# Optimization experiments

Hardware: AMD Instinct MI355X
Metric: run time of the kernel (lower is better)

Reference implementation:

```python
import jax, jax.numpy as jnp
import numpy as np

P_THRESH = 20  # p=0.2 * 100
# direction -> (di, dj): masked pixel (i,j) writes input[i,j] to x[i+di, j+dj], then avg to x[i,j]
OFFSETS = {0: (-1, -1), 1: (-1, 0), 2: (-1, 1), 3: (0, -1), 4: (0, 0), 5: (0, 1), 6: (1, -1), 7: (1, 0)}


def _shift(a, di, dj):
    """out[i+di, j+dj] = a[i, j] on last two axes; out-of-range -> 0/False."""
    H, W = a.shape[-2], a.shape[-1]
    pad = [(0, 0)] * (a.ndim - 2) + [(max(di, 0), max(-di, 0)), (max(dj, 0), max(-dj, 0))]
    p = jnp.pad(a, pad)
    sh, sw = max(-di, 0), max(-dj, 0)
    return p[..., sh:sh + H, sw:sw + W]


def _avg3x3_reflect(x):
    H, W = x.shape[-2], x.shape[-1]
    p = jnp.pad(x, [(0, 0), (0, 0), (1, 1), (1, 1)], mode='reflect')
    s = jnp.zeros_like(x)
    for i in range(3):
        for j in range(3):
            s = s + p[..., i:i + H, j:j + W]
    return s / 9.0


def brown_forward(input, dir, prob):
    avg = _avg3x3_reflect(input)
    pos = prob <= P_THRESH
    x = input
    for d in range(8):  # sequential, matching torch in-place write order
        di, dj = OFFSETS[d]
        m = (dir == d) & pos
        if d == 4:
            x = jnp.where(m, avg, x)  # mm: only avg write
        else:
            sm = _shift(m, di, dj)                       # neighbor-target mask
            x = jnp.where(sm, _shift(input, di, dj), x)  # x[i+di,j+dj] = input[i,j]
            mv = _shift(sm, -di, -dj)                    # mask restricted to valid region
            x = jnp.where(mv, avg, x)                    # x[i,j] = avg[i,j]
    return x


def setup_inputs() -> dict:
    key = jax.random.key(0)
    k1, k2, k3 = jax.random.split(key, 3)
    shape = (32, 64, 128, 128)
    return {
        'input': jax.random.normal(k1, shape, dtype=jnp.float32),
        'dir': jax.random.randint(k2, shape, 0, 8, dtype=jnp.int32),
        'prob': jax.random.randint(k3, shape, 1, 100, dtype=jnp.int32),
    }


def reference(input, dir, prob):
    return brown_forward(input, dir, prob)
```

## Files before the change

### kernel.cpp

```cpp
#include <hip/hip_runtime.h>
#include <cstddef>

#define H 128
#define W 128
#define TILE_R 32
#define P_THRESH 20

__global__ __launch_bounds__(256, 6)
void brown_kernel(const float* __restrict__ inp,
                  const int*  __restrict__ dirp,
                  const int*  __restrict__ prb,
                  float* __restrict__ out)
{
    const int tid   = threadIdx.x;
    const int bid   = blockIdx.x;
    const int slice = bid >> 2;
    const int r0    = (bid & 3) * TILE_R;
    const size_t base = (size_t)slice * (size_t)(H * W);

    const int cq  = tid & 31;
    const int rg  = tid >> 5;
    const int j0  = cq << 2;
    const int gi0 = r0 + (rg << 2);

    auto load_row = [&](int k, float v[6], unsigned& ma, unsigned& mb) {
        const int gr  = gi0 - 1 + k;
        const int gri = (gr < 0) ? 1 : ((gr >= H) ? (H - 2) : gr);
        const float4 c = ((const float4*)(inp + base + (size_t)gri * W))[cq];
        unsigned mwc;
        if ((unsigned)gr < (unsigned)H) {
            const int4 dv = ((const int4*)(dirp + base + (size_t)gr * W))[cq];
            const int4 pv = ((const int4*)(prb  + base + (size_t)gr * W))[cq];
            const unsigned a  = (pv.x <= P_THRESH) ? (unsigned)dv.x : 8u;
            const unsigned b  = (pv.y <= P_THRESH) ? (unsigned)dv.y : 8u;
            const unsigned cc = (pv.z <= P_THRESH) ? (unsigned)dv.z : 8u;
            const unsigned d  = (pv.w <= P_THRESH) ? (unsigned)dv.w : 8u;
            mwc = a | (b << 8) | (cc << 16) | (d << 24);
        } else {
            mwc = 0x08080808u;
        }
        const float    lf  = __shfl_up(c.w, 1);
        const float    rt  = __shfl_down(c.x, 1);
        const unsigned mwl = __shfl_up(mwc, 1);
        const unsigned mwr = __shfl_down(mwc, 1);
        v[1] = c.x; v[2] = c.y; v[3] = c.z; v[4] = c.w;
        v[0] = (cq > 0)  ? lf : c.y;
        v[5] = (cq < 31) ? rt : c.z;
        const unsigned ml = (cq > 0)  ? (mwl >> 24)  : 8u;
        const unsigned mr = (cq < 31) ? (mwr & 255u) : 8u;
        ma = (mwc << 8) | ml;
        mb = (mwc >> 8) | (mr << 24);
    };

    float va[6], vb[6], vc[6];
    unsigned maa, mab, mba, mbb, mca, mcb;
    load_row(0, va, maa, mab);
    load_row(1, vb, mba, mbb);

    #pragma unroll
    for (int rr = 0; rr < 4; ++rr) {
        load_row(rr + 2, vc, mca, mcb);

        const int gi = gi0 + rr;
        float cs[6];
        #pragma unroll
        for (int w = 0; w < 6; ++w) cs[w] = va[w] + vb[w] + vc[w];

        float4 res;
        float* rp = (float*)&res;
        #pragma unroll
        for (int p = 0; p < 4; ++p) {
            const float avg = (cs[p] + cs[p + 1] + cs[p + 2]) * (1.0f / 9.0f);
            const unsigned wTop = (p < 2) ? (maa >> (8 * p)) : (mab >> (8 * (p - 2)));
            const unsigned wMid = (p < 2) ? (mba >> (8 * p)) : (mbb >> (8 * (p - 2)));
            const unsigned wBot = (p < 2) ? (mca >> (8 * p)) : (mcb >> (8 * (p - 2)));

            float val = vb[p + 1];
            int dl = -1;
            if (((wBot >> 16) & 255u) == 0u) { val = vc[p + 2]; dl = 0; }
            if (((wBot >>  8) & 255u) == 1u) { val = vc[p + 1]; dl = 1; }
            if (( wBot        & 255u) == 2u) { val = vc[p];     dl = 2; }
            if (((wMid >> 16) & 255u) == 3u) { val = vb[p + 2]; dl = 3; }
            if (( wMid        & 255u) == 5u) { val = vb[p];     dl = 5; }
            if (((wTop >> 16) & 255u) == 6u) { val = va[p + 2]; dl = 6; }
            if (((wTop >>  8) & 255u) == 7u) { val = va[p + 1]; dl = 7; }

            const int msel = (int)((wMid >> 8) & 255u);
            const int q3 = (msel * 11) >> 5;
            const int di = q3 - 1;
            const int dj = msel - q3 * 3 - 1;
            const int ti = gi + di;
            const int tj = j0 + p + dj;
            const bool bok = (msel < 8) & ((unsigned)ti < 128u) & ((unsigned)tj < 128u);
            if (bok & (msel >= dl)) val = avg;
            rp[p] = val;
        }
        ((float4*)(out + base + (size_t)gi * W))[cq] = res;

        #pragma unroll
        for (int w = 0; w < 6; ++w) { va[w] = vb[w]; vb[w] = vc[w]; }
        maa = mba; mab = mbb; mba = mca; mbb = mcb;
    }
}

extern "C" void kernel_launch(void* const* d_in, const int* in_sizes, int n_in,
                              void* d_out, int out_size, void* d_ws, size_t ws_size,
                              hipStream_t stream) {
    const float* inp  = (const float*)d_in[0];
    const int*   dirp = (const int*)d_in[1];
    const int*   prb  = (const int*)d_in[2];
    float* out = (float*)d_out;

    const int slices = in_sizes[0] / (H * W);
    const int grid = slices * (H / TILE_R);
    brown_kernel<<<grid, 256, 0, stream>>>(inp, dirp, prb, out);
}
```

Measured before the change: 405.6 us.

## Batch all window row loads upfront, use 8 rows per thread and nontemporal stores

Each thread now handles 8 output rows instead of 4, and each block covers 64 rows instead of 32, which cuts the halo re-read overhead from 6/4 to 10/8 rows. All input, dir and prob loads for the 10-row window are issued up front, so more memory requests are in flight before any compute starts. Output is written with nontemporal stores. The cost is higher register pressure (launch bounds lowered to 4 blocks per SM) and half as many blocks in the grid.

Result: faster. 396.0 us (-2.4%).

```diff
diff --git a/kernel.cpp b/kernel.cpp
--- a/kernel.cpp
+++ b/kernel.cpp
@@ -3,10 +3,13 @@
 
 #define H 128
 #define W 128
-#define TILE_R 32
+#define ROWS 8
+#define WIN (ROWS + 2)
 #define P_THRESH 20
 
-__global__ __launch_bounds__(256, 6)
+typedef float nf4 __attribute__((ext_vector_type(4)));
+
+__global__ __launch_bounds__(256, 4)
 void brown_kernel(const float* __restrict__ inp,
                   const int*  __restrict__ dirp,
                   const int*  __restrict__ prb,
@@ -14,20 +17,27 @@
 {
     const int tid   = threadIdx.x;
     const int bid   = blockIdx.x;
-    const int slice = bid >> 2;
-    const int r0    = (bid & 3) * TILE_R;
+    const int slice = bid >> 1;
+    const int r0    = (bid & 1) << 6;
     const size_t base = (size_t)slice * (size_t)(H * W);
 
     const int cq  = tid & 31;
     const int rg  = tid >> 5;
     const int j0  = cq << 2;
-    const int gi0 = r0 + (rg << 2);
+    const int gi0 = r0 + rg * ROWS;
 
-    auto load_row = [&](int k, float v[6], unsigned& ma, unsigned& mb) {
+    float4 c[WIN];
+    #pragma unroll
+    for (int k = 0; k < WIN; ++k) {
         const int gr  = gi0 - 1 + k;
         const int gri = (gr < 0) ? 1 : ((gr >= H) ? (H - 2) : gr);
-        const float4 c = ((const float4*)(inp + base + (size_t)gri * W))[cq];
-        unsigned mwc;
+        c[k] = ((const float4*)(inp + base + (size_t)gri * W))[cq];
+    }
+
+    unsigned mw[WIN];
+    #pragma unroll
+    for (int k = 0; k < WIN; ++k) {
+        const int gr = gi0 - 1 + k;
         if ((unsigned)gr < (unsigned)H) {
             const int4 dv = ((const int4*)(dirp + base + (size_t)gr * W))[cq];
             const int4 pv = ((const int4*)(prb  + base + (size_t)gr * W))[cq];
@@ -35,39 +45,49 @@
             const unsigned b  = (pv.y <= P_THRESH) ? (unsigned)dv.y : 8u;
             const unsigned cc = (pv.z <= P_THRESH) ? (unsigned)dv.z : 8u;
             const unsigned d  = (pv.w <= P_THRESH) ? (unsigned)dv.w : 8u;
-            mwc = a | (b << 8) | (cc << 16) | (d << 24);
+            mw[k] = a | (b << 8) | (cc << 16) | (d << 24);
         } else {
-            mwc = 0x08080808u;
+            mw[k] = 0x08080808u;
         }
-        const float    lf  = __shfl_up(c.w, 1);
-        const float    rt  = __shfl_down(c.x, 1);
-        const unsigned mwl = __shfl_up(mwc, 1);
-        const unsigned mwr = __shfl_down(mwc, 1);
-        v[1] = c.x; v[2] = c.y; v[3] = c.z; v[4] = c.w;
-        v[0] = (cq > 0)  ? lf : c.y;
-        v[5] = (cq < 31) ? rt : c.z;
+    }
+
+    float lf[WIN], rt[WIN];
+    unsigned ma[WIN], mb[WIN];
+    #pragma unroll
+    for (int k = 0; k < WIN; ++k) {
+        const float    l   = __shfl_up(c[k].w, 1);
+        const float    r   = __shfl_down(c[k].x, 1);
+        const unsigned mwl = __shfl_up(mw[k], 1);
+        const unsigned mwr = __shfl_down(mw[k], 1);
+        lf[k] = (cq > 0)  ? l : c[k].y;
+        rt[k] = (cq < 31) ? r : c[k].z;
         const unsigned ml = (cq > 0)  ? (mwl >> 24)  : 8u;
         const unsigned mr = (cq < 31) ? (mwr & 255u) : 8u;
-        ma = (mwc << 8) | ml;
-        mb = (mwc >> 8) | (mr << 24);
-    };
-
-    float va[6], vb[6], vc[6];
-    unsigned maa, mab, mba, mbb, mca, mcb;
-    load_row(0, va, maa, mab);
-    load_row(1, vb, mba, mbb);
+        ma[k] = (mw[k] << 8) | ml;
+        mb[k] = (mw[k] >> 8) | (mr << 24);
+    }
 
     #pragma unroll
-    for (int rr = 0; rr < 4; ++rr) {
-        load_row(rr + 2, vc, mca, mcb);
+    for (int rr = 0; rr < ROWS; ++rr) {
+        const int gi = gi0 + rr;
 
-        const int gi = gi0 + rr;
+        float va[6], vb[6], vc[6];
+        va[0] = lf[rr];     va[1] = c[rr].x;   va[2] = c[rr].y;
+        va[3] = c[rr].z;    va[4] = c[rr].w;   va[5] = rt[rr];
+        vb[0] = lf[rr+1];   vb[1] = c[rr+1].x; vb[2] = c[rr+1].y;
+        vb[3] = c[rr+1].z;  vb[4] = c[rr+1].w; vb[5] = rt[rr+1];
+        vc[0] = lf[rr+2];   vc[1] = c[rr+2].x; vc[2] = c[rr+2].y;
+        vc[3] = c[rr+2].z;  vc[4] = c[rr+2].w; vc[5] = rt[rr+2];
+
         float cs[6];
         #pragma unroll
         for (int w = 0; w < 6; ++w) cs[w] = va[w] + vb[w] + vc[w];
 
-        float4 res;
-        float* rp = (float*)&res;
+        const unsigned maa = ma[rr],   mab = mb[rr];
+        const unsigned mba = ma[rr+1], mbb = mb[rr+1];
+        const unsigned mca = ma[rr+2], mcb = mb[rr+2];
+
+        nf4 res;
         #pragma unroll
         for (int p = 0; p < 4; ++p) {
             const float avg = (cs[p] + cs[p + 1] + cs[p + 2]) * (1.0f / 9.0f);
@@ -93,13 +113,9 @@
             const int tj = j0 + p + dj;
             const bool bok = (msel < 8) & ((unsigned)ti < 128u) & ((unsigned)tj < 128u);
             if (bok & (msel >= dl)) val = avg;
-            rp[p] = val;
+            res[p] = val;
         }
-        ((float4*)(out + base + (size_t)gi * W))[cq] = res;
-
-        #pragma unroll
-        for (int w = 0; w < 6; ++w) { va[w] = vb[w]; vb[w] = vc[w]; }
-        maa = mba; mab = mbb; mba = mca; mbb = mcb;
+        __builtin_nontemporal_store(res, (nf4*)(out + base + (size_t)gi * W) + cq);
     }
 }
 
@@ -112,6 +128,6 @@
     float* out = (float*)d_out;
 
     const int slices = in_sizes[0] / (H * W);
-    const int grid = slices * (H / TILE_R);
+    const int grid = slices * 2;
     brown_kernel<<<grid, 256, 0, stream>>>(inp, dirp, prb, out);
 }
```

## Stage per-wave row tiles in LDS via direct global-to-LDS loads

Applied to the files above, without the earlier changes.

Each wave now loads a 10-row halo tile of input into LDS with global_load_lds and packs the direction/probability masks into LDS, instead of having every thread reload overlapping rows and exchange mask bytes through shuffles. Each half-wave then computes 4 output rows from LDS, and output is written with nontemporal stores. The aim is to cut redundant global reads of halo rows (from 6 loaded rows per 4 output rows down to 10 per 8 per wave) and to issue all loads up front for more memory-level parallelism. In exchange it adds LDS traffic and a wait on all outstanding loads before compute. It also relies on global_load_lds landing data at the expected per-lane offsets with no barrier, which is safe only because each wave reads only its own LDS region.

Measured after the change: 392.6 us. 1.03x faster.

```diff
diff --git a/kernel.cpp b/kernel.cpp
--- a/kernel.cpp
+++ b/kernel.cpp
@@ -3,8 +3,13 @@
 
 #define H 128
 #define W 128
-#define TILE_R 32
+#define WROWS 8
+#define LROWS 10
 #define P_THRESH 20
+
+typedef float nf4 __attribute__((ext_vector_type(4)));
+typedef __attribute__((address_space(1))) const unsigned int glo_u32;
+typedef __attribute__((address_space(3))) unsigned int lds_u32;
 
 __global__ __launch_bounds__(256, 6)
 void brown_kernel(const float* __restrict__ inp,
@@ -12,37 +17,71 @@
                   const int*  __restrict__ prb,
                   float* __restrict__ out)
 {
+    __shared__ __align__(16) float s_in[4 * LROWS * W];
+    __shared__ unsigned int        s_mk[4 * LROWS * 32];
+
     const int tid   = threadIdx.x;
+    const int wid   = tid >> 6;
+    const int lane  = tid & 63;
     const int bid   = blockIdx.x;
     const int slice = bid >> 2;
-    const int r0    = (bid & 3) * TILE_R;
+    const int r0    = (bid & 3) << 5;
+    const int wr0   = r0 + wid * WROWS;
     const size_t base = (size_t)slice * (size_t)(H * W);
 
-    const int cq  = tid & 31;
-    const int rg  = tid >> 5;
-    const int j0  = cq << 2;
-    const int gi0 = r0 + (rg << 2);
+    float*        s_in_w = s_in + wid * (LROWS * W);
+    unsigned int* s_mk_w = s_mk + wid * (LROWS * 32);
 
-    auto load_row = [&](int k, float v[6], unsigned& ma, unsigned& mb) {
-        const int gr  = gi0 - 1 + k;
+    int4 dvv[5], pvv[5];
+    #pragma unroll
+    for (int w = 0; w < 5; ++w) {
+        const int idx = w * 64 + lane;
+        const int L   = idx >> 5;
+        const int c4  = idx & 31;
+        const int gr  = wr0 - 1 + L;
+        if ((unsigned)gr < (unsigned)H) {
+            dvv[w] = ((const int4*)(dirp + base + (size_t)gr * W))[c4];
+            pvv[w] = ((const int4*)(prb  + base + (size_t)gr * W))[c4];
+        } else {
+            dvv[w] = make_int4(8, 8, 8, 8);
+            pvv[w] = make_int4(100, 100, 100, 100);
+        }
+    }
+    #pragma unroll
+    for (int w = 0; w < 5; ++w) {
+        const int idx = w * 64 + lane;
+        const int L   = idx >> 5;
+        const int c4  = idx & 31;
+        const int gr  = wr0 - 1 + L;
         const int gri = (gr < 0) ? 1 : ((gr >= H) ? (H - 2) : gr);
-        const float4 c = ((const float4*)(inp + base + (size_t)gri * W))[cq];
-        unsigned mwc;
-        if ((unsigned)gr < (unsigned)H) {
-            const int4 dv = ((const int4*)(dirp + base + (size_t)gr * W))[cq];
-            const int4 pv = ((const int4*)(prb  + base + (size_t)gr * W))[cq];
-            const unsigned a  = (pv.x <= P_THRESH) ? (unsigned)dv.x : 8u;
-            const unsigned b  = (pv.y <= P_THRESH) ? (unsigned)dv.y : 8u;
-            const unsigned cc = (pv.z <= P_THRESH) ? (unsigned)dv.z : 8u;
-            const unsigned d  = (pv.w <= P_THRESH) ? (unsigned)dv.w : 8u;
-            mwc = a | (b << 8) | (cc << 16) | (d << 24);
-        } else {
-            mwc = 0x08080808u;
-        }
-        const float    lf  = __shfl_up(c.w, 1);
-        const float    rt  = __shfl_down(c.x, 1);
-        const unsigned mwl = __shfl_up(mwc, 1);
-        const unsigned mwr = __shfl_down(mwc, 1);
+        const float* gp = inp + base + (size_t)gri * W + c4 * 4;
+        __builtin_amdgcn_global_load_lds((glo_u32*)gp, (lds_u32*)(s_in_w + idx * 4), 16, 0, 0);
+    }
+    #pragma unroll
+    for (int w = 0; w < 5; ++w) {
+        const int idx = w * 64 + lane;
+        const unsigned a  = (pvv[w].x <= P_THRESH) ? (unsigned)dvv[w].x : 8u;
+        const unsigned b  = (pvv[w].y <= P_THRESH) ? (unsigned)dvv[w].y : 8u;
+        const unsigned cc = (pvv[w].z <= P_THRESH) ? (unsigned)dvv[w].z : 8u;
+        const unsigned d  = (pvv[w].w <= P_THRESH) ? (unsigned)dvv[w].w : 8u;
+        s_mk_w[idx] = a | (b << 8) | (cc << 16) | (d << 24);
+    }
+    asm volatile("s_waitcnt vmcnt(0)" ::: "memory");
+
+    const int cq   = lane & 31;
+    const int rh   = lane >> 6 ? 0 : (lane >> 5);
+    const int j0   = cq << 2;
+    const int lrb  = rh << 2;
+    const int cqm1 = (cq > 0)  ? cq - 1 : 0;
+    const int cqp1 = (cq < 31) ? cq + 1 : 31;
+
+    auto load_row = [&](int L, float v[6], unsigned& ma, unsigned& mb) {
+        const float4   c   = ((const float4*)(s_in_w + L * W))[cq];
+        const unsigned mwc = s_mk_w[L * 32 + cq];
+        const unsigned mwl = s_mk_w[L * 32 + cqm1];
+        const unsigned mwr = s_mk_w[L * 32 + cqp1];
+        const float lf = __shfl_up(c.w, 1);
+        const float rt = __shfl_down(c.x, 1);
         v[1] = c.x; v[2] = c.y; v[3] = c.z; v[4] = c.w;
         v[0] = (cq > 0)  ? lf : c.y;
         v[5] = (cq < 31) ? rt : c.z;
@@ -54,20 +93,19 @@
 
     float va[6], vb[6], vc[6];
     unsigned maa, mab, mba, mbb, mca, mcb;
-    load_row(0, va, maa, mab);
-    load_row(1, vb, mba, mbb);
+    load_row(lrb + 0, va, maa, mab);
+    load_row(lrb + 1, vb, mba, mbb);
 
     #pragma unroll
     for (int rr = 0; rr < 4; ++rr) {
-        load_row(rr + 2, vc, mca, mcb);
+        load_row(lrb + rr + 2, vc, mca, mcb);
 
-        const int gi = gi0 + rr;
+        const int gi = wr0 + (rh << 2) + rr;
         float cs[6];
         #pragma unroll
         for (int w = 0; w < 6; ++w) cs[w] = va[w] + vb[w] + vc[w];
 
-        float4 res;
-        float* rp = (float*)&res;
+        nf4 res;
         #pragma unroll
         for (int p = 0; p < 4; ++p) {
             const float avg = (cs[p] + cs[p + 1] + cs[p + 2]) * (1.0f / 9.0f);
@@ -93,9 +131,9 @@
             const int tj = j0 + p + dj;
             const bool bok = (msel < 8) & ((unsigned)ti < 128u) & ((unsigned)tj < 128u);
             if (bok & (msel >= dl)) val = avg;
-            rp[p] = val;
+            res[p] = val;
         }
-        ((float4*)(out + base + (size_t)gi * W))[cq] = res;
+        __builtin_nontemporal_store(res, (nf4*)(out + base + (size_t)gi * W) + cq);
 
         #pragma unroll
         for (int w = 0; w < 6; ++w) { va[w] = vb[w]; vb[w] = vc[w]; }
@@ -112,6 +150,6 @@
     float* out = (float*)d_out;
 
     const int slices = in_sizes[0] / (H * W);
-    const int grid = slices * (H / TILE_R);
+    const int grid = slices * 4;
     brown_kernel<<<grid, 256, 0, stream>>>(inp, dirp, prb, out);
 }
```

## Compute one row per wavefront with overlapping unaligned loads instead of shuffles

Applied to the files above, without the earlier changes.

The kernel now assigns each 64-lane wavefront a single output row, with each lane producing two pixels. Each lane loads unaligned 4-wide windows of the three neighbouring rows directly from memory, replacing the shuffle-based halo exchange and the rolling 4-row register pipeline. Image-edge validity is folded into the mask bytes up front, so the per-pixel bounds check goes away. In exchange, every input, direction and probability element is read about three times per row neighbourhood, and the unaligned vector loads rely on L1/L2 to absorb the redundant traffic. The grid grows eightfold to compensate.

After: 397.2 us. 1.02x faster.

```diff
diff --git a/kernel.cpp b/kernel.cpp
--- a/kernel.cpp
+++ b/kernel.cpp
@@ -3,8 +3,11 @@
 
 #define H 128
 #define W 128
-#define TILE_R 32
 #define P_THRESH 20
+
+typedef float f4u __attribute__((ext_vector_type(4), aligned(4)));
+typedef int   i4u __attribute__((ext_vector_type(4), aligned(4)));
+typedef float nf2 __attribute__((ext_vector_type(2)));
 
 __global__ __launch_bounds__(256, 6)
 void brown_kernel(const float* __restrict__ inp,
@@ -12,95 +15,116 @@
                   const int*  __restrict__ prb,
                   float* __restrict__ out)
 {
-    const int tid   = threadIdx.x;
-    const int bid   = blockIdx.x;
-    const int slice = bid >> 2;
-    const int r0    = (bid & 3) * TILE_R;
+    const int tid  = threadIdx.x;
+    const int lane = tid & 63;
+    const int bid  = blockIdx.x;
+    const int slice = bid >> 5;
+    const int gi   = ((bid & 31) << 2) | (tid >> 6);
     const size_t base = (size_t)slice * (size_t)(H * W);
 
-    const int cq  = tid & 31;
-    const int rg  = tid >> 5;
-    const int j0  = cq << 2;
-    const int gi0 = r0 + (rg << 2);
+    const int j0 = lane << 1;
+    const int cl = (lane == 0) ? 0 : ((lane == 63) ? (W - 4) : (j0 - 1));
 
-    auto load_row = [&](int k, float v[6], unsigned& ma, unsigned& mb) {
-        const int gr  = gi0 - 1 + k;
-        const int gri = (gr < 0) ? 1 : ((gr >= H) ? (H - 2) : gr);
-        const float4 c = ((const float4*)(inp + base + (size_t)gri * W))[cq];
-        unsigned mwc;
-        if ((unsigned)gr < (unsigned)H) {
-            const int4 dv = ((const int4*)(dirp + base + (size_t)gr * W))[cq];
-            const int4 pv = ((const int4*)(prb  + base + (size_t)gr * W))[cq];
-            const unsigned a  = (pv.x <= P_THRESH) ? (unsigned)dv.x : 8u;
-            const unsigned b  = (pv.y <= P_THRESH) ? (unsigned)dv.y : 8u;
-            const unsigned cc = (pv.z <= P_THRESH) ? (unsigned)dv.z : 8u;
-            const unsigned d  = (pv.w <= P_THRESH) ? (unsigned)dv.w : 8u;
-            mwc = a | (b << 8) | (cc << 16) | (d << 24);
-        } else {
-            mwc = 0x08080808u;
+    const int rT = (gi == 0) ? 1 : gi - 1;
+    const int rB = (gi == H - 1) ? H - 2 : gi + 1;
+
+    const float* ip = inp  + base;
+    const int*   dp = dirp + base;
+    const int*   pp = prb  + base;
+
+    const f4u iT = *(const f4u*)(ip + (size_t)rT * W + cl);
+    const f4u iM = *(const f4u*)(ip + (size_t)gi * W + cl);
+    const f4u iB = *(const f4u*)(ip + (size_t)rB * W + cl);
+    const i4u dT = *(const i4u*)(dp + (size_t)rT * W + cl);
+    const i4u dM = *(const i4u*)(dp + (size_t)gi * W + cl);
+    const i4u dB = *(const i4u*)(dp + (size_t)rB * W + cl);
+    const i4u pT = *(const i4u*)(pp + (size_t)rT * W + cl);
+    const i4u pM = *(const i4u*)(pp + (size_t)gi * W + cl);
+    const i4u pB = *(const i4u*)(pp + (size_t)rB * W + cl);
+
+    auto packm = [](i4u d, i4u p) -> unsigned {
+        const unsigned a = (p.x <= P_THRESH) ? (unsigned)d.x : 8u;
+        const unsigned b = (p.y <= P_THRESH) ? (unsigned)d.y : 8u;
+        const unsigned c = (p.z <= P_THRESH) ? (unsigned)d.z : 8u;
+        const unsigned e = (p.w <= P_THRESH) ? (unsigned)d.w : 8u;
+        return a | (b << 8) | (c << 16) | (e << 24);
+    };
+    unsigned mT = packm(dT, pT);
+    unsigned mM = packm(dM, pM);
+    unsigned mB = packm(dB, pB);
+
+    if (gi == 0) {
+        mT = 0x08080808u;
+        unsigned r = 0;
+        #pragma unroll
+        for (int i2 = 0; i2 < 4; ++i2) {
+            unsigned b = (mM >> (8 * i2)) & 255u;
+            b = (b <= 2u) ? 8u : b;
+            r |= b << (8 * i2);
         }
-        const float    lf  = __shfl_up(c.w, 1);
-        const float    rt  = __shfl_down(c.x, 1);
-        const unsigned mwl = __shfl_up(mwc, 1);
-        const unsigned mwr = __shfl_down(mwc, 1);
-        v[1] = c.x; v[2] = c.y; v[3] = c.z; v[4] = c.w;
-        v[0] = (cq > 0)  ? lf : c.y;
-        v[5] = (cq < 31) ? rt : c.z;
-        const unsigned ml = (cq > 0)  ? (mwl >> 24)  : 8u;
-        const unsigned mr = (cq < 31) ? (mwr & 255u) : 8u;
-        ma = (mwc << 8) | ml;
-        mb = (mwc >> 8) | (mr << 24);
-    };
+        mM = r;
+    } else if (gi == H - 1) {
+        mB = 0x08080808u;
+        unsigned r = 0;
+        #pragma unroll
+        for (int i2 = 0; i2 < 4; ++i2) {
+            unsigned b = (mM >> (8 * i2)) & 255u;
+            b = (b >= 6u) ? 8u : b;
+            r |= b << (8 * i2);
+        }
+        mM = r;
+    }
 
-    float va[6], vb[6], vc[6];
-    unsigned maa, mab, mba, mbb, mca, mcb;
-    load_row(0, va, maa, mab);
-    load_row(1, vb, mba, mbb);
+    float vT[4] = {iT.x, iT.y, iT.z, iT.w};
+    float vM[4] = {iM.x, iM.y, iM.z, iM.w};
+    float vB[4] = {iB.x, iB.y, iB.z, iB.w};
+    if (lane == 0) {
+        vT[0] = iT.y; vT[1] = iT.x; vT[2] = iT.y; vT[3] = iT.z;
+        vM[0] = iM.y; vM[1] = iM.x; vM[2] = iM.y; vM[3] = iM.z;
+        vB[0] = iB.y; vB[1] = iB.x; vB[2] = iB.y; vB[3] = iB.z;
+        mT = (mT << 8) | 8u;
+        mB = (mB << 8) | 8u;
+        mM = (mM << 8) | 8u;
+        const unsigned b1 = (mM >> 8) & 255u;
+        if ((0x49u >> b1) & 1u) mM = (mM & ~0xFF00u) | (8u << 8);
+    } else if (lane == 63) {
+        vT[0] = iT.y; vT[1] = iT.z; vT[2] = iT.w; vT[3] = iT.z;
+        vM[0] = iM.y; vM[1] = iM.z; vM[2] = iM.w; vM[3] = iM.z;
+        vB[0] = iB.y; vB[1] = iB.z; vB[2] = iB.w; vB[3] = iB.z;
+        mT = (mT >> 8) | 0x08000000u;
+        mB = (mB >> 8) | 0x08000000u;
+        mM = (mM >> 8) | 0x08000000u;
+        const unsigned b2 = (mM >> 16) & 255u;
+        if ((0x24u >> b2) & 1u) mM = (mM & ~0xFF0000u) | (8u << 16);
+    }
 
+    float cs[4];
     #pragma unroll
-    for (int rr = 0; rr < 4; ++rr) {
-        load_row(rr + 2, vc, mca, mcb);
+    for (int w = 0; w < 4; ++w) cs[w] = vT[w] + vM[w] + vB[w];
 
-        const int gi = gi0 + rr;
-        float cs[6];
-        #pragma unroll
-        for (int w = 0; w < 6; ++w) cs[w] = va[w] + vb[w] + vc[w];
+    nf2 res;
+    #pragma unroll
+    for (int p = 0; p < 2; ++p) {
+        const float avg = (cs[p] + cs[p + 1] + cs[p + 2]) * (1.0f / 9.0f);
+        const unsigned wT = mT >> (8 * p);
+        const unsigned wM = mM >> (8 * p);
+        const unsigned wB = mB >> (8 * p);
 
-        float4 res;
-        float* rp = (float*)&res;
-        #pragma unroll
-        for (int p = 0; p < 4; ++p) {
-            const float avg = (cs[p] + cs[p + 1] + cs[p + 2]) * (1.0f / 9.0f);
-            const unsigned wTop = (p < 2) ? (maa >> (8 * p)) : (mab >> (8 * (p - 2)));
-            const unsigned wMid = (p < 2) ? (mba >> (8 * p)) : (mbb >> (8 * (p - 2)));
-            const unsigned wBot = (p < 2) ? (mca >> (8 * p)) : (mcb >> (8 * (p - 2)));
+        float val = vM[p + 1];
+        int dl = -1;
+        if (((wB >> 16) & 255u) == 0u) { val = vB[p + 2]; dl = 0; }
+        if (((wB >>  8) & 255u) == 1u) { val = vB[p + 1]; dl = 1; }
+        if (( wB        & 255u) == 2u) { val = vB[p];     dl = 2; }
+        if (((wM >> 16) & 255u) == 3u) { val = vM[p + 2]; dl = 3; }
+        if (( wM        & 255u) == 5u) { val = vM[p];     dl = 5; }
+        if (((wT >> 16) & 255u) == 6u) { val = vT[p + 2]; dl = 6; }
+        if (((wT >>  8) & 255u) == 7u) { val = vT[p + 1]; dl = 7; }
 
-            float val = vb[p + 1];
-            int dl = -1;
-            if (((wBot >> 16) & 255u) == 0u) { val = vc[p + 2]; dl = 0; }
-            if (((wBot >>  8) & 255u) == 1u) { val = vc[p + 1]; dl = 1; }
-            if (( wBot        & 255u) == 2u) { val = vc[p];     dl = 2; }
-            if (((wMid >> 16) & 255u) == 3u) { val = vb[p + 2]; dl = 3; }
-            if (( wMid        & 255u) == 5u) { val = vb[p];     dl = 5; }
-            if (((wTop >> 16) & 255u) == 6u) { val = va[p + 2]; dl = 6; }
-            if (((wTop >>  8) & 255u) == 7u) { val = va[p + 1]; dl = 7; }
-
-            const int msel = (int)((wMid >> 8) & 255u);
-            const int q3 = (msel * 11) >> 5;
-            const int di = q3 - 1;
-            const int dj = msel - q3 * 3 - 1;
-            const int ti = gi + di;
-            const int tj = j0 + p + dj;
-            const bool bok = (msel < 8) & ((unsigned)ti < 128u) & ((unsigned)tj < 128u);
-            if (bok & (msel >= dl)) val = avg;
-            rp[p] = val;
-        }
-        ((float4*)(out + base + (size_t)gi * W))[cq] = res;
-
-        #pragma unroll
-        for (int w = 0; w < 6; ++w) { va[w] = vb[w]; vb[w] = vc[w]; }
-        maa = mba; mab = mbb; mba = mca; mbb = mcb;
+        const int msel = (int)((wM >> 8) & 255u);
+        if ((msel < 8) & (msel >= dl)) val = avg;
+        res[p] = val;
     }
+    *(nf2*)(out + base + (size_t)gi * W + j0) = res;
 }
 
 extern "C" void kernel_launch(void* const* d_in, const int* in_sizes, int n_in,
@@ -112,6 +136,6 @@
     float* out = (float*)d_out;
 
     const int slices = in_sizes[0] / (H * W);
-    const int grid = slices * (H / TILE_R);
+    const int grid = slices * 32;
     brown_kernel<<<grid, 256, 0, stream>>>(inp, dirp, prb, out);
 }
```
